# Kernel optimization log

Hardware: AMD Instinct MI355X
Metric: run time of the kernel (lower is better)

Reference implementation:

```python
import jax, jax.numpy as jnp
import numpy as np

NUM_ITERS = 3

def squash(t, axis):
    # scale = |t|^2/(1+|t|^2); out = scale * t / |t|
    sn = jnp.sum(t * t, axis=axis, keepdims=True)
    return (sn / (1.0 + sn)) * t / jnp.sqrt(sn)


def setup_inputs() -> dict:
    key = jax.random.key(0)
    k1, k2, k3, k4 = jax.random.split(key, 4)
    B = 128
    inputs = jax.random.normal(k1, (B, 256, 20, 20), dtype=jnp.float32)
    conv_w = jax.random.normal(k2, (8, 32, 256, 9, 9), dtype=jnp.float32) * 0.05
    conv_b = jax.random.normal(k3, (8, 32), dtype=jnp.float32) * 0.05
    route_weights = jax.random.normal(k4, (10, 1152, 8, 16), dtype=jnp.float32)
    return {"inputs": inputs, "conv_w": conv_w, "conv_b": conv_b,
            "route_weights": route_weights}


def reference(inputs, conv_w, conv_b, route_weights):
    B = inputs.shape[0]
    K, O, Cin, kh, kw = conv_w.shape          # 8 capsules, 32 out-chans each
    # --- primary capsules: 8 parallel convs fused into one grouped-output conv ---
    w = conv_w.reshape(K * O, Cin, kh, kw)
    out = jax.lax.conv_general_dilated(
        inputs, w, window_strides=(2, 2), padding='VALID',
        dimension_numbers=('NCHW', 'OIHW', 'NCHW'))  # [B, K*O, 6, 6]
    out = out + conv_b.reshape(K * O)[None, :, None, None]
    H = out.shape[-1]
    x = out.reshape(B, K, O * H * H).transpose(0, 2, 1)  # [B, 1152, 8]
    x = squash(x, axis=2)
    # --- routing layer ---
    # prediction_vectors: x[None,:,:,None,:] @ W[:,None,:,:,:] -> [10,B,1152,1,16]
    pred = jnp.einsum('bri,crio->cbro', x, route_weights)[:, :, :, None, :]
    logits = jnp.zeros_like(pred)
    v = None
    for i in range(NUM_ITERS):
        # routing_softmax(dim=2): softmax over the routes axis (faithful to source)
        c = jax.nn.softmax(logits, axis=2)
        s = jnp.sum(c * pred, axis=2, keepdims=True)  # [10,B,1,1,16]
        v = squash(s, axis=1)                          # squash default dim=1 (batch) -- faithful
        if i != NUM_ITERS - 1:
            logits = logits + jnp.sum(pred * v, axis=-1, keepdims=True)
    # [10,B,1,1,16] -> squeeze -> [10,B,16] -> permute(1,0,2) -> [B,10,16]
    return jnp.squeeze(v).transpose(1, 0, 2)
```

## Files before the change

kernel.cpp:

```cpp
#include <hip/hip_runtime.h>
#include <math.h>

typedef _Float16 f16;
typedef _Float16 f16x4 __attribute__((ext_vector_type(4)));
typedef _Float16 f16x8 __attribute__((ext_vector_type(8)));
typedef float f32x4 __attribute__((ext_vector_type(4)));
typedef float f32x8 __attribute__((ext_vector_type(8)));

#define AS1 __attribute__((address_space(1)))
#define AS3 __attribute__((address_space(3)))

__device__ __forceinline__ void gld_lds16(const f16* g, f16* l) {
#if defined(__has_builtin) && __has_builtin(__builtin_amdgcn_global_load_lds)
    __builtin_amdgcn_global_load_lds((const AS1 void*)g, (AS3 void*)l, 16, 0, 0);
#else
    *(uint4*)l = *(const uint4*)g;
#endif
}

__global__ __launch_bounds__(256) void mega_pre3(
    const float* __restrict__ inp, f16* __restrict__ in_t,
    const float* __restrict__ cw,  f16* __restrict__ w_t,
    const float* __restrict__ rw,  f16* __restrict__ rwh,
    float* __restrict__ s0)
{
    __shared__ __align__(16) char smem[27 * 258 * 2];
    const int bx = blockIdx.x, tid = threadIdx.x;

    if (bx < 13312) {
        const int b = bx & 127, c0 = ((bx >> 7) & 7) * 32, p0 = (bx >> 10) * 32;
        const int tx = tid & 31, ty = tid >> 5;
        float (*t)[33] = (float(*)[33])smem;
#pragma unroll
        for (int j = 0; j < 4; ++j) {
            int c = ty + j * 8, p = p0 + tx;
            if (p < 400) t[c][tx] = inp[((size_t)b * 256 + c0 + c) * 400 + p];
        }
        __syncthreads();
#pragma unroll
        for (int j = 0; j < 4; ++j) {
            int p = p0 + ty + j * 8;
            if (p < 400) in_t[((size_t)b * 400 + p) * 256 + c0 + tx] = (f16)t[tx][ty + j * 8];
        }
    } else if (bx < 14080) {
        const int q = bx - 13312, n = q / 3, cc = q - n * 3;
        f16* buf = (f16*)smem;
        const float* src = cw + (size_t)n * 20736 + cc * 27;
        for (int i = tid; i < 27 * 256; i += 256) {
            int cin = i / 27, pp = i - cin * 27;
            buf[pp * 258 + cin] = (f16)src[cin * 81 + pp];
        }
        __syncthreads();
        f16* dst = w_t + (size_t)n * 20736 + cc * 27 * 256;
        for (int j = tid; j < 27 * 256; j += 256) {
            int pl = j >> 8, cin = j & 255;
            dst[j] = buf[pl * 258 + cin];
        }
    } else if (bx < 15520) {
        int g = (bx - 14080) * 256 + tid;
        int cr = g >> 5, rem = g & 31;
        int o = rem >> 1, h = (rem & 1) * 4;
        const float* src = rw + (size_t)cr * 128 + o;
        f16x4 v;
#pragma unroll
        for (int j = 0; j < 4; ++j) v[j] = (f16)src[(h + j) * 16];
        *(f16x4*)(rwh + (size_t)cr * 128 + o * 8 + h) = v;
    } else {
        int idx = (bx - 15520) * 256 + tid;
        ((float4*)s0)[idx] = make_float4(0.f, 0.f, 0.f, 0.f);
    }
}

#define SPLITK 14
__global__ __launch_bounds__(256, 2) void conv_mfma(
    const f16* __restrict__ in_t,
    const f16* __restrict__ w_t,
    f16* __restrict__ part)
{
    __shared__ f16 As[3][128 * 32];
    __shared__ f16 Bs[3][256 * 32];
    const int tid = threadIdx.x;
    const int lane = tid & 63, wave = tid >> 6;
    const int wm = wave >> 1, wn = wave & 1;

    const int bid = blockIdx.x + 36 * blockIdx.z;
    const int wgid = (bid & 7) * 63 + (bid >> 3);
    const int m0 = (wgid % 36) * 128;
    const int kz = wgid / 36;

    const int kc0 = kz * 46 + (kz < 4 ? kz : 4);
    const int NT  = (kz < 4) ? 47 : 46;

    int srcA[2], srcB[4];
#pragma unroll
    for (int i = 0; i < 2; ++i) {
        int pairp = i * 32 + (tid >> 3);
        int chunk8 = (tid & 7) ^ (pairp & 7);
        int e = chunk8 >> 2, q4 = chunk8 & 3;
        int m = m0 + pairp * 2 + e;
        int b = m / 36, hw = m - b * 36;
        int ho = hw / 6, wo = hw - ho * 6;
        srcA[i] = ((b * 20 + 2 * ho) * 20 + 2 * wo) * 256 + q4 * 8;
    }
#pragma unroll
    for (int i = 0; i < 4; ++i) {
        int pairp = i * 32 + (tid >> 3);
        int chunk8 = (tid & 7) ^ (pairp & 7);
        int e = chunk8 >> 2, q4 = chunk8 & 3;
        int n = pairp * 2 + e;
        srcB[i] = n * 20736 + q4 * 8;
    }

    const int row = lane & 15, quad = lane >> 4;
    int offA[4], offB[8];
#pragma unroll
    for (int mt = 0; mt < 4; ++mt) {
        int m = wm * 64 + mt * 16 + row;
        int ph8 = (((m & 1) << 2) + quad) ^ ((m >> 1) & 7);
        offA[mt] = (m >> 1) * 64 + ph8 * 8;
    }
#pragma unroll
    for (int nt = 0; nt < 8; ++nt) {
        int n = wn * 128 + nt * 16 + row;
        int ph8 = (((n & 1) << 2) + quad) ^ ((n >> 1) & 7);
        offB[nt] = (n >> 1) * 64 + ph8 * 8;
    }

    f32x4 acc[4][8] = {};

#define KOFFS(T) int kc = kc0 + (T); int pp = kc >> 3, cq = kc & 7;           \
    int kh = pp / 9, kw = pp - kh * 9;                                        \
    int koffA = (kh * 20 + kw) * 256 + cq * 32; int koffB = kc * 32;
#define STAGE1(T, BUF) do { KOFFS(T)                                          \
        gld_lds16(in_t + srcA[0] + koffA, &As[BUF][tid * 8]);                 \
        gld_lds16(in_t + srcA[1] + koffA, &As[BUF][2048 + tid * 8]);          \
        gld_lds16(w_t + srcB[0] + koffB, &Bs[BUF][tid * 8]);                  \
    } while (0)
#define STAGE2(T, BUF) do { KOFFS(T)                                          \
        gld_lds16(w_t + srcB[1] + koffB, &Bs[BUF][2048 + tid * 8]);           \
        gld_lds16(w_t + srcB[2] + koffB, &Bs[BUF][4096 + tid * 8]);           \
        gld_lds16(w_t + srcB[3] + koffB, &Bs[BUF][6144 + tid * 8]);           \
    } while (0)

    STAGE1(0, 0); STAGE2(0, 0);
    STAGE1(1, 1); STAGE2(1, 1);
    asm volatile("s_waitcnt vmcnt(6)" ::: "memory");
    __builtin_amdgcn_s_barrier();

    int buf = 0;
    for (int t = 0; t < NT; ++t) {
        const f16* Ab = &As[buf][0];
        const f16* Bb = &Bs[buf][0];
        int bn = buf + 2; if (bn >= 3) bn -= 3;
        f16x8 af[4], bfr[8];

#pragma unroll
        for (int mt = 0; mt < 4; ++mt) af[mt] = *(const f16x8*)(Ab + offA[mt]);
#pragma unroll
        for (int nt = 0; nt < 4; ++nt) bfr[nt] = *(const f16x8*)(Bb + offB[nt]);
        if (t + 2 < NT) STAGE1(t + 2, bn);
        __builtin_amdgcn_s_barrier();
        asm volatile("s_waitcnt lgkmcnt(0)" ::: "memory");
        __builtin_amdgcn_sched_barrier(0);
        __builtin_amdgcn_s_setprio(1);
#pragma unroll
        for (int mt = 0; mt < 4; ++mt)
#pragma unroll
            for (int nt = 0; nt < 4; ++nt)
                acc[mt][nt] = __builtin_amdgcn_mfma_f32_16x16x32_f16(
                    af[mt], bfr[nt], acc[mt][nt], 0, 0, 0);
        __builtin_amdgcn_s_setprio(0);
        __builtin_amdgcn_s_barrier();

#pragma unroll
        for (int nt = 4; nt < 8; ++nt) bfr[nt] = *(const f16x8*)(Bb + offB[nt]);
        if (t + 2 < NT) STAGE2(t + 2, bn);
        if (t + 2 < NT)
            asm volatile("s_waitcnt vmcnt(6)" ::: "memory");
        else if (t + 1 < NT)
            asm volatile("s_waitcnt vmcnt(0)" ::: "memory");
        __builtin_amdgcn_s_barrier();
        asm volatile("s_waitcnt lgkmcnt(0)" ::: "memory");
        __builtin_amdgcn_sched_barrier(0);
        __builtin_amdgcn_s_setprio(1);
#pragma unroll
        for (int mt = 0; mt < 4; ++mt)
#pragma unroll
            for (int nt = 4; nt < 8; ++nt)
                acc[mt][nt] = __builtin_amdgcn_mfma_f32_16x16x32_f16(
                    af[mt], bfr[nt], acc[mt][nt], 0, 0, 0);
        __builtin_amdgcn_s_setprio(0);
        __builtin_amdgcn_s_barrier();

        if (++buf == 3) buf = 0;
    }
#undef STAGE1
#undef STAGE2
#undef KOFFS

    const int col = lane & 15, qr = (lane >> 4) * 4;
    f16* pb = part + (size_t)kz * 4608 * 256;
#pragma unroll
    for (int mt = 0; mt < 4; ++mt)
#pragma unroll
        for (int rg = 0; rg < 4; ++rg) {
            int m = m0 + wm * 64 + mt * 16 + qr + rg;
#pragma unroll
            for (int nt = 0; nt < 8; ++nt) {
                int n = wn * 128 + nt * 16 + col;
                pb[(size_t)m * 256 + n] = (f16)acc[mt][nt][rg];
            }
        }
}

__global__ __launch_bounds__(256) void combine_squash4(
    const f16* __restrict__ part, const float* __restrict__ bias,
    f16* __restrict__ xh)
{
    int idx = blockIdx.x * 256 + threadIdx.x;
    int g = idx & 7, si = (idx >> 3) & 3, m = idx >> 5;
    int b = m / 36, hw = m - b * 36;
    int sbeg = si * 4, scnt = (si < 3) ? 4 : 2;

    float val[8][4] = {};
    for (int s2 = 0; s2 < scnt; ++s2) {
        const f16* p = part + ((size_t)(sbeg + s2) * 4608 + m) * 256 + g * 4;
#pragma unroll
        for (int k = 0; k < 8; ++k) {
            f16x4 v = *(const f16x4*)(p + k * 32);
#pragma unroll
            for (int j = 0; j < 4; ++j) val[k][j] += (float)v[j];
        }
    }
#pragma unroll
    for (int k = 0; k < 8; ++k)
#pragma unroll
        for (int j = 0; j < 4; ++j) {
            val[k][j] += __shfl_xor(val[k][j], 8);
            val[k][j] += __shfl_xor(val[k][j], 16);
        }
    if (si == 0) {
#pragma unroll
        for (int j = 0; j < 4; ++j) {
            float sn = 0.f;
            float vb[8];
#pragma unroll
            for (int k = 0; k < 8; ++k) {
                vb[k] = val[k][j] + bias[k * 32 + g * 4 + j];
                sn += vb[k] * vb[k];
            }
            float scale = sqrtf(sn) / (1.f + sn);
            int r = (g * 4 + j) * 36 + hw;
            f16x8 hv;
#pragma unroll
            for (int k = 0; k < 8; ++k) hv[k] = (f16)(vb[k] * scale);
            *(f16x8*)(xh + ((size_t)b * 1152 + r) * 8) = hv;
        }
    }
}

__global__ __launch_bounds__(256) void pred_s0h(
    const f16* __restrict__ xh,
    const f16* __restrict__ rwh,
    f16* __restrict__ pred,
    float* __restrict__ s0)
{
    const int c = blockIdx.x, r0 = blockIdx.y * 32, b0 = blockIdx.z * 32;
    const int tid = threadIdx.x;
    const int o = tid & 15, rp = tid >> 4;
    const int r = r0 + rp * 2;

    __shared__ float s_sh[32 * 16];
    s_sh[tid] = 0.f; s_sh[tid + 256] = 0.f;

    f16x8 w0h = *(const f16x8*)(rwh + ((size_t)(c * 1152 + r) * 16 + o) * 8);
    f16x8 w1h = *(const f16x8*)(rwh + ((size_t)(c * 1152 + r + 1) * 16 + o) * 8);
    f32x8 W0 = __builtin_convertvector(w0h, f32x8);
    f32x8 W1 = __builtin_convertvector(w1h, f32x8);
    __syncthreads();

    for (int bb = 0; bb < 32; bb += 2) {
        const int ba = b0 + bb, bc = b0 + bb + 1;
        f16x8 xa0 = *(const f16x8*)(xh + ((size_t)ba * 1152 + r) * 8);
        f16x8 xa1 = *(const f16x8*)(xh + ((size_t)ba * 1152 + r + 1) * 8);
        f16x8 xc0 = *(const f16x8*)(xh + ((size_t)bc * 1152 + r) * 8);
        f16x8 xc1 = *(const f16x8*)(xh + ((size_t)bc * 1152 + r + 1) * 8);
        f32x8 A0 = __builtin_convertvector(xa0, f32x8);
        f32x8 A1 = __builtin_convertvector(xa1, f32x8);
        f32x8 C0 = __builtin_convertvector(xc0, f32x8);
        f32x8 C1 = __builtin_convertvector(xc1, f32x8);
        float pa0 = A0[0]*W0[0] + A0[1]*W0[1] + A0[2]*W0[2] + A0[3]*W0[3]
                  + A0[4]*W0[4] + A0[5]*W0[5] + A0[6]*W0[6] + A0[7]*W0[7];
        float pa1 = A1[0]*W1[0] + A1[1]*W1[1] + A1[2]*W1[2] + A1[3]*W1[3]
                  + A1[4]*W1[4] + A1[5]*W1[5] + A1[6]*W1[6] + A1[7]*W1[7];
        float pc0 = C0[0]*W0[0] + C0[1]*W0[1] + C0[2]*W0[2] + C0[3]*W0[3]
                  + C0[4]*W0[4] + C0[5]*W0[5] + C0[6]*W0[6] + C0[7]*W0[7];
        float pc1 = C1[0]*W1[0] + C1[1]*W1[1] + C1[2]*W1[2] + C1[3]*W1[3]
                  + C1[4]*W1[4] + C1[5]*W1[5] + C1[6]*W1[6] + C1[7]*W1[7];
        f16* pba = pred + ((size_t)(c * 128 + ba) * 1152 + r) * 16 + o;
        f16* pbc = pred + ((size_t)(c * 128 + bc) * 1152 + r) * 16 + o;
        pba[0]  = (f16)pa0;  pba[16] = (f16)pa1;
        pbc[0]  = (f16)pc0;  pbc[16] = (f16)pc1;
        float psa = pa0 + pa1, psc = pc0 + pc1;
        psa += __shfl_xor(psa, 16); psc += __shfl_xor(psc, 16);
        psa += __shfl_xor(psa, 32); psc += __shfl_xor(psc, 32);
        if ((tid & 63) < 16) {
            atomicAdd(&s_sh[bb * 16 + o], psa);
            atomicAdd(&s_sh[(bb + 1) * 16 + o], psc);
        }
    }
    __syncthreads();
    for (int i = tid; i < 512; i += 256) {
        int bb = i >> 4, oo = i & 15;
        atomicAdd(&s0[((size_t)c * 128 + b0 + bb) * 16 + oo], s_sh[i]);
    }
}

__global__ __launch_bounds__(256) void route_f16v(
    const f16* __restrict__ pred,
    const float* __restrict__ sa, const float* __restrict__ za,
    const float* __restrict__ sb2, const float* __restrict__ zb2,
    float* __restrict__ s_out,
    float* __restrict__ z_out)
{
    const int c = blockIdx.x, b = blockIdx.y, tid = threadIdx.x;
    const size_t base = (size_t)(c * 128 + b) * 1152;
    const int o = tid & 15, seg = tid >> 4;

    __shared__ float lred[16][17];
    __shared__ float vs[16];

#define VSADD(S, Z) do {                                                      \
        float part_ = 0.f;                                                    \
        _Pragma("unroll")                                                     \
        for (int j = 0; j < 8; ++j) {                                         \
            int bb = seg * 8 + j;                                             \
            float zin = (Z) ? 1.f / (Z)[c * 128 + bb] : (1.f / 1152.f);       \
            float q = (S)[((size_t)c * 128 + bb) * 16 + o] * zin;             \
            part_ += q * q;                                                   \
        }                                                                     \
        lred[seg][o] = part_;                                                 \
        __syncthreads();                                                      \
        if (tid < 16) {                                                       \
            float t_ = 0.f;                                                   \
            _Pragma("unroll")                                                 \
            for (int i = 0; i < 16; ++i) t_ += lred[i][tid];                  \
            float zin = (Z) ? 1.f / (Z)[c * 128 + b] : (1.f / 1152.f);        \
            vs[tid] += (S)[((size_t)c * 128 + b) * 16 + tid] * zin *          \
                       sqrtf(t_) / (1.f + t_);                                \
        }                                                                     \
        __syncthreads();                                                      \
    } while (0)

    if (tid < 16) vs[tid] = 0.f;
    __syncthreads();
    VSADD(sa, za);
    if (sb2) VSADD(sb2, zb2);
#undef VSADD

    float vr[16];
#pragma unroll
    for (int j = 0; j < 16; ++j) vr[j] = vs[j];

    float sacc[16];
#pragma unroll
    for (int j = 0; j < 16; ++j) sacc[j] = 0.f;
    float zacc = 0.f;

    for (int r = tid; r < 1152; r += 256) {
        const f16x8* pp = (const f16x8*)(pred + (base + r) * 16);
        f32x8 q0 = __builtin_convertvector(pp[0], f32x8);
        f32x8 q1 = __builtin_convertvector(pp[1], f32x8);
        float t = 0.f;
#pragma unroll
        for (int j = 0; j < 8; ++j) t += q0[j] * vr[j] + q1[j] * vr[j + 8];
        float e = __expf(t);
#pragma unroll
        for (int j = 0; j < 8; ++j) { sacc[j] += e * q0[j]; sacc[j + 8] += e * q1[j]; }
        zacc += e;
    }

    __shared__ float red[256][16];
    __shared__ float red2[16][16];
    __shared__ float zred[256];
    __shared__ float zpart[16];
#pragma unroll
    for (int j = 0; j < 16; ++j) red[tid][j] = sacc[j];
    zred[tid] = zacc;
    __syncthreads();
    {
        float t = 0.f;
#pragma unroll
        for (int j = 0; j < 16; ++j) t += red[seg * 16 + j][o];
        red2[seg][o] = t;
        if (tid < 16) {
            float tz = 0.f;
#pragma unroll
            for (int j = 0; j < 16; ++j) tz += zred[tid * 16 + j];
            zpart[tid] = tz;
        }
    }
    __syncthreads();
    if (tid < 16) {
        float t = 0.f;
#pragma unroll
        for (int sg = 0; sg < 16; ++sg) t += red2[sg][tid];
        s_out[(size_t)(c * 128 + b) * 16 + tid] = t;
    } else if (tid == 16) {
        float tz = 0.f;
#pragma unroll
        for (int j = 0; j < 16; ++j) tz += zpart[j];
        z_out[c * 128 + b] = tz;
    }
}

__global__ __launch_bounds__(128) void squash_final(
    const float* __restrict__ s, const float* __restrict__ z,
    float* __restrict__ out)
{
    const int c = blockIdx.x, b = threadIdx.x;
    float sv[16];
    const float* sp = s + ((size_t)c * 128 + b) * 16;
    float zin = 1.f / z[c * 128 + b];
#pragma unroll
    for (int o = 0; o < 16; ++o) sv[o] = sp[o] * zin;
    __shared__ float m[16][129];
#pragma unroll
    for (int o = 0; o < 16; ++o) m[o][b] = sv[o] * sv[o];
    __syncthreads();
    __shared__ float sn[16];
    if (b < 16) {
        float t = 0.f;
        for (int i = 0; i < 128; ++i) t += m[b][i];
        sn[b] = t;
    }
    __syncthreads();
#pragma unroll
    for (int o = 0; o < 16; ++o) {
        float scale = sqrtf(sn[o]) / (1.f + sn[o]);
        out[((size_t)b * 10 + c) * 16 + o] = sv[o] * scale;
    }
}

extern "C" void kernel_launch(void* const* d_in, const int* in_sizes, int n_in,
                              void* d_out, int out_size, void* d_ws, size_t ws_size,
                              hipStream_t stream)
{
    (void)in_sizes; (void)n_in; (void)out_size; (void)ws_size;
    const float* inp = (const float*)d_in[0];
    const float* cw  = (const float*)d_in[1];
    const float* cb  = (const float*)d_in[2];
    const float* rw  = (const float*)d_in[3];
    float* out = (float*)d_out;

    char* ws = (char*)d_ws;
    f16*   part = (f16*)(ws);
    f16*   pred = (f16*)(ws);
    f16*   in_t = (f16*)(ws + 33030144);
    f16*   w_t  = (f16*)(ws + 59244544);
    f16*   rwh  = (f16*)(ws + 69861376);
    f16*   xh   = (f16*)(ws + 72810496);
    float* s0   = (float*)(ws + 75169792);
    float* sB   = (float*)(ws + 75251712);
    float* sC   = (float*)(ws + 75333632);
    float* zB   = (float*)(ws + 75415552);
    float* zC   = (float*)(ws + 75420672);

    mega_pre3<<<15540, 256, 0, stream>>>(inp, in_t, cw, w_t, rw, rwh, s0);

    conv_mfma<<<dim3(36, 1, SPLITK), 256, 0, stream>>>(in_t, w_t, part);
    combine_squash4<<<576, 256, 0, stream>>>(part, cb, xh);

    pred_s0h<<<dim3(10, 36, 4), 256, 0, stream>>>(xh, rwh, pred, s0);

    route_f16v<<<dim3(10, 128), 256, 0, stream>>>(pred, s0, nullptr, nullptr, nullptr,
                                                  sB, zB);
    route_f16v<<<dim3(10, 128), 256, 0, stream>>>(pred, s0, nullptr, sB, zB,
                                                  sC, zC);
    squash_final<<<10, 128, 0, stream>>>(sC, zC, out);
}
```

Measured before the change: 233.9 us.

## Fuse combine, prediction, routing and final squash into one cooperative kernel

Replaces five separate launches (combine/squash, prediction, two routing passes, final squash) with a single cooperative kernel of 1440 blocks that uses grid-wide syncs between phases, keeping the old launches as a fallback if cooperative launch fails. The goal is to remove launch gaps and per-kernel tail effects. The prediction phase also changes from two batch elements per iteration to one, with shared memory aliased across phases. The cost is grid.sync overhead, a cap of 6 blocks per CU from the launch bounds, and idle blocks in the phases that use fewer than 1440 blocks.

```diff
diff --git a/kernel.cpp b/kernel.cpp
--- a/kernel.cpp
+++ b/kernel.cpp
@@ -1,5 +1,8 @@
 #include <hip/hip_runtime.h>
+#include <hip/hip_cooperative_groups.h>
 #include <math.h>
+
+namespace cg = cooperative_groups;
 
 typedef _Float16 f16;
 typedef _Float16 f16x4 __attribute__((ext_vector_type(4)));
@@ -213,18 +216,19 @@
         }
 }
 
-__global__ __launch_bounds__(256) void combine_squash4(
+
+__device__ __forceinline__ void combine_body(
     const f16* __restrict__ part, const float* __restrict__ bias,
-    f16* __restrict__ xh)
-{
-    int idx = blockIdx.x * 256 + threadIdx.x;
+    f16* __restrict__ xh, int bid, int tid)
+{
+    int idx = bid * 256 + tid;
     int g = idx & 7, si = (idx >> 3) & 3, m = idx >> 5;
     int b = m / 36, hw = m - b * 36;
     int sbeg = si * 4, scnt = (si < 3) ? 4 : 2;
 
     float val[8][4] = {};
-    for (int s2 = 0; s2 < scnt; ++s2) {
-        const f16* p = part + ((size_t)(sbeg + s2) * 4608 + m) * 256 + g * 4;
+    for (int s2i = 0; s2i < scnt; ++s2i) {
+        const f16* p = part + ((size_t)(sbeg + s2i) * 4608 + m) * 256 + g * 4;
 #pragma unroll
         for (int k = 0; k < 8; ++k) {
             f16x4 v = *(const f16x4*)(p + k * 32);
@@ -259,18 +263,14 @@
     }
 }
 
-__global__ __launch_bounds__(256) void pred_s0h(
-    const f16* __restrict__ xh,
-    const f16* __restrict__ rwh,
-    f16* __restrict__ pred,
-    float* __restrict__ s0)
-{
-    const int c = blockIdx.x, r0 = blockIdx.y * 32, b0 = blockIdx.z * 32;
-    const int tid = threadIdx.x;
+__device__ __forceinline__ void pred_body(
+    const f16* __restrict__ xh, const f16* __restrict__ rwh,
+    f16* __restrict__ pred, float* __restrict__ s0,
+    int c, int r0, int b0, int tid, float* s_sh)
+{
     const int o = tid & 15, rp = tid >> 4;
     const int r = r0 + rp * 2;
 
-    __shared__ float s_sh[32 * 16];
     s_sh[tid] = 0.f; s_sh[tid + 256] = 0.f;
 
     f16x8 w0h = *(const f16x8*)(rwh + ((size_t)(c * 1152 + r) * 16 + o) * 8);
@@ -279,35 +279,23 @@
     f32x8 W1 = __builtin_convertvector(w1h, f32x8);
     __syncthreads();
 
-    for (int bb = 0; bb < 32; bb += 2) {
-        const int ba = b0 + bb, bc = b0 + bb + 1;
-        f16x8 xa0 = *(const f16x8*)(xh + ((size_t)ba * 1152 + r) * 8);
-        f16x8 xa1 = *(const f16x8*)(xh + ((size_t)ba * 1152 + r + 1) * 8);
-        f16x8 xc0 = *(const f16x8*)(xh + ((size_t)bc * 1152 + r) * 8);
-        f16x8 xc1 = *(const f16x8*)(xh + ((size_t)bc * 1152 + r + 1) * 8);
-        f32x8 A0 = __builtin_convertvector(xa0, f32x8);
-        f32x8 A1 = __builtin_convertvector(xa1, f32x8);
-        f32x8 C0 = __builtin_convertvector(xc0, f32x8);
-        f32x8 C1 = __builtin_convertvector(xc1, f32x8);
-        float pa0 = A0[0]*W0[0] + A0[1]*W0[1] + A0[2]*W0[2] + A0[3]*W0[3]
-                  + A0[4]*W0[4] + A0[5]*W0[5] + A0[6]*W0[6] + A0[7]*W0[7];
-        float pa1 = A1[0]*W1[0] + A1[1]*W1[1] + A1[2]*W1[2] + A1[3]*W1[3]
-                  + A1[4]*W1[4] + A1[5]*W1[5] + A1[6]*W1[6] + A1[7]*W1[7];
-        float pc0 = C0[0]*W0[0] + C0[1]*W0[1] + C0[2]*W0[2] + C0[3]*W0[3]
-                  + C0[4]*W0[4] + C0[5]*W0[5] + C0[6]*W0[6] + C0[7]*W0[7];
-        float pc1 = C1[0]*W1[0] + C1[1]*W1[1] + C1[2]*W1[2] + C1[3]*W1[3]
-                  + C1[4]*W1[4] + C1[5]*W1[5] + C1[6]*W1[6] + C1[7]*W1[7];
-        f16* pba = pred + ((size_t)(c * 128 + ba) * 1152 + r) * 16 + o;
-        f16* pbc = pred + ((size_t)(c * 128 + bc) * 1152 + r) * 16 + o;
-        pba[0]  = (f16)pa0;  pba[16] = (f16)pa1;
-        pbc[0]  = (f16)pc0;  pbc[16] = (f16)pc1;
-        float psa = pa0 + pa1, psc = pc0 + pc1;
-        psa += __shfl_xor(psa, 16); psc += __shfl_xor(psc, 16);
-        psa += __shfl_xor(psa, 32); psc += __shfl_xor(psc, 32);
-        if ((tid & 63) < 16) {
-            atomicAdd(&s_sh[bb * 16 + o], psa);
-            atomicAdd(&s_sh[(bb + 1) * 16 + o], psc);
-        }
+    for (int bb = 0; bb < 32; ++bb) {
+        const int b = b0 + bb;
+        f16x8 x0h = *(const f16x8*)(xh + ((size_t)b * 1152 + r) * 8);
+        f16x8 x1h = *(const f16x8*)(xh + ((size_t)b * 1152 + r + 1) * 8);
+        f32x8 X0 = __builtin_convertvector(x0h, f32x8);
+        f32x8 X1 = __builtin_convertvector(x1h, f32x8);
+        float p0 = X0[0]*W0[0] + X0[1]*W0[1] + X0[2]*W0[2] + X0[3]*W0[3]
+                 + X0[4]*W0[4] + X0[5]*W0[5] + X0[6]*W0[6] + X0[7]*W0[7];
+        float p1 = X1[0]*W1[0] + X1[1]*W1[1] + X1[2]*W1[2] + X1[3]*W1[3]
+                 + X1[4]*W1[4] + X1[5]*W1[5] + X1[6]*W1[6] + X1[7]*W1[7];
+        f16* pb = pred + ((size_t)(c * 128 + b) * 1152 + r) * 16 + o;
+        pb[0]  = (f16)p0;
+        pb[16] = (f16)p1;
+        float ps = p0 + p1;
+        ps += __shfl_xor(ps, 16);
+        ps += __shfl_xor(ps, 32);
+        if ((tid & 63) < 16) atomicAdd(&s_sh[bb * 16 + o], ps);
     }
     __syncthreads();
     for (int i = tid; i < 512; i += 256) {
@@ -316,19 +304,25 @@
     }
 }
 
-__global__ __launch_bounds__(256) void route_f16v(
+__device__ __forceinline__ void route_body(
     const f16* __restrict__ pred,
     const float* __restrict__ sa, const float* __restrict__ za,
     const float* __restrict__ sb2, const float* __restrict__ zb2,
-    float* __restrict__ s_out,
-    float* __restrict__ z_out)
-{
-    const int c = blockIdx.x, b = blockIdx.y, tid = threadIdx.x;
+    float* __restrict__ s_out, float* __restrict__ z_out,
+    int c, int b, int tid, char* sm)
+{
     const size_t base = (size_t)(c * 128 + b) * 1152;
     const int o = tid & 15, seg = tid >> 4;
 
-    __shared__ float lred[16][17];
-    __shared__ float vs[16];
+    float (*red)[16]  = (float(*)[16])sm;
+    float (*red2)[16] = (float(*)[16])(sm + 16384);
+    float* zred  = (float*)(sm + 17408);
+    float* zpart = (float*)(sm + 18432);
+    float (*lred)[17] = (float(*)[17])sm;
+    float* vs    = (float*)(sm + 18496);
+
+    if (tid < 16) vs[tid] = 0.f;
+    __syncthreads();
 
 #define VSADD(S, Z) do {                                                      \
         float part_ = 0.f;                                                    \
@@ -352,8 +346,6 @@
         __syncthreads();                                                      \
     } while (0)
 
-    if (tid < 16) vs[tid] = 0.f;
-    __syncthreads();
     VSADD(sa, za);
     if (sb2) VSADD(sb2, zb2);
 #undef VSADD
@@ -361,6 +353,7 @@
     float vr[16];
 #pragma unroll
     for (int j = 0; j < 16; ++j) vr[j] = vs[j];
+    __syncthreads();
 
     float sacc[16];
 #pragma unroll
@@ -380,10 +373,6 @@
         zacc += e;
     }
 
-    __shared__ float red[256][16];
-    __shared__ float red2[16][16];
-    __shared__ float zred[256];
-    __shared__ float zpart[16];
 #pragma unroll
     for (int j = 0; j < 16; ++j) red[tid][j] = sacc[j];
     zred[tid] = zacc;
@@ -412,6 +401,92 @@
         for (int j = 0; j < 16; ++j) tz += zpart[j];
         z_out[c * 128 + b] = tz;
     }
+}
+
+__global__ __launch_bounds__(256, 6) void mega_route(
+    const f16* __restrict__ part, const float* __restrict__ bias,
+    f16* __restrict__ xh, const f16* __restrict__ rwh,
+    f16* __restrict__ pred, float* __restrict__ s0,
+    float* __restrict__ s1, float* __restrict__ z1,
+    float* __restrict__ s2, float* __restrict__ z2,
+    float* __restrict__ out)
+{
+    cg::grid_group grid = cg::this_grid();
+    const int bid = blockIdx.x, tid = threadIdx.x;
+    __shared__ __align__(16) char sm[18560];
+
+    if (bid < 576) combine_body(part, bias, xh, bid, tid);
+    grid.sync();
+
+    {
+        const int c = bid / 144, rem = bid - c * 144;
+        pred_body(xh, rwh, pred, s0, c, (rem >> 2) * 32, (rem & 3) * 32, tid, (float*)sm);
+    }
+    grid.sync();
+
+    if (bid < 1280) route_body(pred, s0, nullptr, nullptr, nullptr, s1, z1,
+                               bid >> 7, bid & 127, tid, sm);
+    grid.sync();
+
+    if (bid < 1280) route_body(pred, s0, nullptr, s1, z1, s2, z2,
+                               bid >> 7, bid & 127, tid, sm);
+    grid.sync();
+
+    if (bid < 10) {
+        const int c = bid;
+        const bool act = tid < 128;
+        const int b = tid & 127;
+        float (*m)[129] = (float(*)[129])sm;
+        float* sn = (float*)(sm + 8256);
+        float sv[16];
+        if (act) {
+            float zin = 1.f / z2[c * 128 + b];
+            const float* sp = s2 + ((size_t)c * 128 + b) * 16;
+#pragma unroll
+            for (int o = 0; o < 16; ++o) { sv[o] = sp[o] * zin; m[o][b] = sv[o] * sv[o]; }
+        }
+        __syncthreads();
+        if (tid < 16) {
+            float t = 0.f;
+            for (int i = 0; i < 128; ++i) t += m[tid][i];
+            sn[tid] = t;
+        }
+        __syncthreads();
+        if (act) {
+#pragma unroll
+            for (int o = 0; o < 16; ++o) {
+                float scale = sqrtf(sn[o]) / (1.f + sn[o]);
+                out[((size_t)b * 10 + c) * 16 + o] = sv[o] * scale;
+            }
+        }
+    }
+}
+
+__global__ __launch_bounds__(256) void combine_squash4(
+    const f16* __restrict__ part, const float* __restrict__ bias,
+    f16* __restrict__ xh)
+{
+    combine_body(part, bias, xh, blockIdx.x, threadIdx.x);
+}
+
+__global__ __launch_bounds__(256) void pred_s0h(
+    const f16* __restrict__ xh, const f16* __restrict__ rwh,
+    f16* __restrict__ pred, float* __restrict__ s0)
+{
+    __shared__ float s_sh[512];
+    pred_body(xh, rwh, pred, s0, blockIdx.x, blockIdx.y * 32, blockIdx.z * 32,
+              threadIdx.x, s_sh);
+}
+
+__global__ __launch_bounds__(256) void route_f16v(
+    const f16* __restrict__ pred,
+    const float* __restrict__ sa, const float* __restrict__ za,
+    const float* __restrict__ sb2, const float* __restrict__ zb2,
+    float* __restrict__ s_out, float* __restrict__ z_out)
+{
+    __shared__ __align__(16) char sm[18560];
+    route_body(pred, sa, za, sb2, zb2, s_out, z_out, blockIdx.x, blockIdx.y,
+               threadIdx.x, sm);
 }
 
 __global__ __launch_bounds__(128) void squash_final(
@@ -467,15 +542,20 @@
     float* zC   = (float*)(ws + 75420672);
 
     mega_pre3<<<15540, 256, 0, stream>>>(inp, in_t, cw, w_t, rw, rwh, s0);
-
     conv_mfma<<<dim3(36, 1, SPLITK), 256, 0, stream>>>(in_t, w_t, part);
-    combine_squash4<<<576, 256, 0, stream>>>(part, cb, xh);
-
-    pred_s0h<<<dim3(10, 36, 4), 256, 0, stream>>>(xh, rwh, pred, s0);
-
-    route_f16v<<<dim3(10, 128), 256, 0, stream>>>(pred, s0, nullptr, nullptr, nullptr,
-                                                  sB, zB);
-    route_f16v<<<dim3(10, 128), 256, 0, stream>>>(pred, s0, nullptr, sB, zB,
-                                                  sC, zC);
-    squash_final<<<10, 128, 0, stream>>>(sC, zC, out);
-}
+
+    void* args[] = {(void*)&part, (void*)&cb, (void*)&xh, (void*)&rwh, (void*)&pred,
+                    (void*)&s0, (void*)&sB, (void*)&zB, (void*)&sC, (void*)&zC,
+                    (void*)&out};
+    hipError_t err = hipLaunchCooperativeKernel((void*)mega_route, dim3(1440), dim3(256),
+                                                args, 0, stream);
+    if (err != hipSuccess) {
+        combine_squash4<<<576, 256, 0, stream>>>(part, cb, xh);
+        pred_s0h<<<dim3(10, 36, 4), 256, 0, stream>>>(xh, rwh, pred, s0);
+        route_f16v<<<dim3(10, 128), 256, 0, stream>>>(pred, s0, nullptr, nullptr, nullptr,
+                                                      sB, zB);
+        route_f16v<<<dim3(10, 128), 256, 0, stream>>>(pred, s0, nullptr, sB, zB,
+                                                      sC, zC);
+        squash_final<<<10, 128, 0, stream>>>(sC, zC, out);
+    }
+}
```

Result: slower. 867.5 us (+271.0%).
